# Kernel tuning notes

Measured on AMD Instinct MI355X. Metric: run time of the kernel, lower is better.

The kernel has to match this reference:

```python
import jax, jax.numpy as jnp
import numpy as np

EPS = 1e-5

def layer_norm(x, w):
    mu = jnp.mean(x, axis=-1, keepdims=True)
    var = jnp.mean((x - mu) ** 2, axis=-1, keepdims=True)
    return (x - mu) * jax.lax.rsqrt(var + EPS) * w

def timestep_embedding(t, dim=256, max_period=10000.0):
    half = dim // 2
    freqs = jnp.exp(-np.log(max_period) * jnp.arange(half, dtype=jnp.float32) / half)
    args = t[:, None].astype(jnp.float32) * freqs[None]
    return jnp.concatenate([jnp.cos(args), jnp.sin(args)], axis=-1)  # (B, dim)


def setup_inputs() -> dict:
    key = jax.random.key(0)
    ks = jax.random.split(key, 16)
    B, S, D, H, L, V, C, F = 2, 1024, 768, 12, 12, 50258, 768, 256
    MLP = 4 * D
    w = 0.02  # init scale for weights
    return {
        "indices": jax.random.randint(ks[0], (B, S), 0, V, dtype=jnp.int32),
        "sigma": jax.random.uniform(ks[1], (B,), dtype=jnp.float32),
        "embed": jax.random.normal(ks[2], (V, D), jnp.float32) * w,
        "t_w1": jax.random.normal(ks[3], (C, F), jnp.float32) * w,
        "t_b1": jnp.zeros((C,), jnp.float32),
        "t_w2": jax.random.normal(ks[4], (C, C), jnp.float32) * w,
        "t_b2": jnp.zeros((C,), jnp.float32),
        "norm1_w": jnp.ones((L, D), jnp.float32),
        "qkv_w": jax.random.normal(ks[5], (L, 3 * D, D), jnp.float32) * w,
        "out_w": jax.random.normal(ks[6], (L, D, D), jnp.float32) * w,
        "norm2_w": jnp.ones((L, D), jnp.float32),
        "mlp_w1": jax.random.normal(ks[7], (L, MLP, D), jnp.float32) * w,
        "mlp_b1": jnp.zeros((L, MLP), jnp.float32),
        "mlp_w2": jax.random.normal(ks[8], (L, D, MLP), jnp.float32) * w,
        "mlp_b2": jnp.zeros((L, D), jnp.float32),
        "ada_w": jax.random.normal(ks[9], (L, 6 * D, C), jnp.float32) * w,
        "ada_b": jnp.zeros((L, 6 * D), jnp.float32),
        "normf_w": jnp.ones((D,), jnp.float32),
        "lin_w": jax.random.normal(ks[10], (V, D), jnp.float32) * w,
        "lin_b": jnp.zeros((V,), jnp.float32),
        "adaf_w": jax.random.normal(ks[11], (2 * D, C), jnp.float32) * w,
        "adaf_b": jnp.zeros((2 * D,), jnp.float32),
    }


def reference(indices, sigma, embed, t_w1, t_b1, t_w2, t_b2, norm1_w, qkv_w,
              out_w, norm2_w, mlp_w1, mlp_b1, mlp_w2, mlp_b2, ada_w, ada_b,
              normf_w, lin_w, lin_b, adaf_w, adaf_b):
    B, S = indices.shape
    D = embed.shape[1]
    L = qkv_w.shape[0]
    H = 12
    dh = D // H
    scale = 1.0 / np.sqrt(dh)

    x = embed[indices]  # (B, S, D)
    # conditioning: c = silu(MLP(sinusoidal(sigma)))
    tf = timestep_embedding(sigma)
    temb = jax.nn.silu(tf @ t_w1.T + t_b1) @ t_w2.T + t_b2
    c = jax.nn.silu(temb)  # (B, C)

    # NOTE: rotary cos/sin are computed but never applied in the original block.
    for l in range(L):
        ada = (c @ ada_w[l].T + ada_b[l]).reshape(B, 6, 1, D)
        sh_msa, sc_msa, g_msa = ada[:, 0], ada[:, 1], ada[:, 2]  # (B, 1, D)
        sh_mlp, sc_mlp, g_mlp = ada[:, 3], ada[:, 4], ada[:, 5]

        xm = layer_norm(x, norm1_w[l]) * (1 + sc_msa) + sh_msa
        qkv = (xm @ qkv_w[l].T).reshape(B, S, 3, H, dh)
        q, k, v = qkv[:, :, 0], qkv[:, :, 1], qkv[:, :, 2]  # (B, S, H, dh)
        attn = jnp.einsum('bqhd,bkhd->bhqk', q, k) * scale
        attn = jax.nn.softmax(attn, axis=-1)
        o = jnp.einsum('bhqk,bkhd->bqhd', attn, v).reshape(B, S, D)
        x = x + g_msa * (o @ out_w[l].T)

        xm = layer_norm(x, norm2_w[l]) * (1 + sc_mlp) + sh_mlp
        h = jax.nn.gelu(xm @ mlp_w1[l].T + mlp_b1[l], approximate=True)
        x = x + g_mlp * (h @ mlp_w2[l].T + mlp_b2[l])

    ada = (c @ adaf_w.T + adaf_b).reshape(B, 2, 1, D)
    shift, sc = ada[:, 0], ada[:, 1]
    xm = layer_norm(x, normf_w) * (1 + sc) + shift
    return xm @ lin_w.T + lin_b  # (B, S, V) log-scores
```

## Files before the change

### kernel.cpp

```cpp
#include <hip/hip_runtime.h>
#include <hip/hip_bf16.h>
#include <math.h>
#include <stdint.h>

typedef __hip_bfloat16 bf16;
typedef __attribute__((ext_vector_type(8))) short bf16x8;
typedef __attribute__((ext_vector_type(4))) float f32x4;

#define DEV_INLINE __device__ __forceinline__

DEV_INLINE float wred_sum(float v) {
    #pragma unroll
    for (int o = 32; o > 0; o >>= 1) v += __shfl_xor(v, o);
    return v;
}
DEV_INLINE float red16_max(float v) {
    v = fmaxf(v, __shfl_xor(v, 1)); v = fmaxf(v, __shfl_xor(v, 2));
    v = fmaxf(v, __shfl_xor(v, 4)); v = fmaxf(v, __shfl_xor(v, 8));
    return v;
}
DEV_INLINE float red16_sum(float v) {
    v += __shfl_xor(v, 1); v += __shfl_xor(v, 2);
    v += __shfl_xor(v, 4); v += __shfl_xor(v, 8);
    return v;
}
DEV_INLINE float gelu_tanh(float v) {
    float t = tanhf(0.7978845608028654f * (v + 0.044715f * v * v * v));
    return 0.5f * v * (1.f + t);
}
DEV_INLINE float silu(float v) { return v / (1.f + expf(-v)); }
DEV_INLINE short f2bs(float f) { bf16 h = __float2bfloat16(f); short s; __builtin_memcpy(&s, &h, 2); return s; }

typedef const __attribute__((address_space(1))) uint32_t* gptr_t;
typedef __attribute__((address_space(3))) uint32_t* lptr_t;

DEV_INLINE void gload_lds16(const bf16* gp, bf16* lp) {
    __builtin_amdgcn_global_load_lds((gptr_t)gp, (lptr_t)lp, 16, 0, 0);
}

DEV_INLINE int xcd_swz(int wg, int nwg) {
    int q = nwg >> 3, r = nwg & 7;
    int xcd = wg & 7, pos = wg >> 3;
    return (xcd < r ? xcd * (q + 1) : r * (q + 1) + (xcd - r) * q) + pos;
}

__global__ void cvt_bf16(const float* __restrict__ in, bf16* __restrict__ out, long n) {
    long i = ((long)blockIdx.x * blockDim.x + threadIdx.x) * 8;
    if (i >= n) return;
    float4 a = *(const float4*)(in + i);
    float4 b = *(const float4*)(in + i + 4);
    bf16x8 v;
    v[0] = f2bs(a.x); v[1] = f2bs(a.y); v[2] = f2bs(a.z); v[3] = f2bs(a.w);
    v[4] = f2bs(b.x); v[5] = f2bs(b.y); v[6] = f2bs(b.z); v[7] = f2bs(b.w);
    *(bf16x8*)(out + i) = v;
}

__global__ void embed_gather(const int* __restrict__ idx,
                             const float* __restrict__ embed,
                             float* __restrict__ x) {
    int i = blockIdx.x * blockDim.x + threadIdx.x;
    int m = i / 192, d4 = i % 192;
    ((float4*)x)[(size_t)m * 192 + d4] =
        ((const float4*)embed)[(size_t)idx[m] * 192 + d4];
}

__global__ void tstep_embed(const float* __restrict__ sigma, float* __restrict__ tf) {
    int t = threadIdx.x;
    int b = t >> 7, i = t & 127;
    float freq = expf(-9.210340371976184f * (float)i / 128.f);
    float a = sigma[b] * freq;
    tf[b * 256 + i]       = cosf(a);
    tf[b * 256 + 128 + i] = sinf(a);
}

template <int ACT>
__global__ void gemm_rowvec(const float* __restrict__ A, const float* __restrict__ W,
                            const float* __restrict__ bias, float* __restrict__ C,
                            int M, int N, int K) {
    int wid  = (int)((blockIdx.x * (size_t)blockDim.x + threadIdx.x) >> 6);
    int lane = threadIdx.x & 63;
    if (wid >= M * N) return;
    int m = wid / N, n = wid % N;
    const float* a = A + (size_t)m * K;
    const float* w = W + (size_t)n * K;
    float s = 0.f;
    for (int k = lane; k < K; k += 64) s = fmaf(a[k], w[k], s);
    s = wred_sum(s);
    if (lane == 0) {
        if (bias) s += bias[n];
        if (ACT == 2) s = silu(s);
        C[wid] = s;
    }
}

__global__ void ada_all(const float* __restrict__ c, const float* __restrict__ ada_w,
                        const float* __restrict__ ada_b, float* __restrict__ out) {
    const int C = 768, SIXD = 4608, B = 2;
    int wid  = (int)((blockIdx.x * (size_t)blockDim.x + threadIdx.x) >> 6);
    int lane = threadIdx.x & 63;
    if (wid >= 12 * B * SIXD) return;
    int j = wid % SIXD;
    int lb = wid / SIXD;
    int b = lb % B, l = lb / B;
    const float* a = c + (size_t)b * C;
    const float* w = ada_w + ((size_t)l * SIXD + j) * C;
    float s = 0.f;
    for (int k = lane; k < C; k += 64) s = fmaf(a[k], w[k], s);
    s = wred_sum(s);
    if (lane == 0) out[wid] = s + ada_b[l * SIXD + j];
}

__global__ __launch_bounds__(256) void ln_mod(const float* __restrict__ x,
                                              const float* __restrict__ w,
                                              const float* __restrict__ sc,
                                              const float* __restrict__ sh,
                                              int bstride,
                                              bf16* __restrict__ out) {
    int r = blockIdx.x;
    int b = r >> 10;
    const float* xr = x + (size_t)r * 768;
    int tid = threadIdx.x, lane = tid & 63, wv = tid >> 6;
    float v0 = xr[tid], v1 = xr[tid + 256], v2 = xr[tid + 512];
    __shared__ float redA[4], redB[4];
    float s = wred_sum(v0 + v1 + v2);
    if (lane == 0) redA[wv] = s;
    __syncthreads();
    float mu = (redA[0] + redA[1] + redA[2] + redA[3]) * (1.f / 768.f);
    float d0 = v0 - mu, d1 = v1 - mu, d2 = v2 - mu;
    float vs = wred_sum(d0 * d0 + d1 * d1 + d2 * d2);
    if (lane == 0) redB[wv] = vs;
    __syncthreads();
    float var  = (redB[0] + redB[1] + redB[2] + redB[3]) * (1.f / 768.f);
    float rstd = rsqrtf(var + 1e-5f);
    const float* scb = sc + (size_t)b * bstride;
    const float* shb = sh + (size_t)b * bstride;
    bf16* outr = out + (size_t)r * 768;
    outr[tid]       = __float2bfloat16(d0 * rstd * w[tid]       * (1.f + scb[tid])       + shb[tid]);
    outr[tid + 256] = __float2bfloat16(d1 * rstd * w[tid + 256] * (1.f + scb[tid + 256]) + shb[tid + 256]);
    outr[tid + 512] = __float2bfloat16(d2 * rstd * w[tid + 512] * (1.f + scb[tid + 512]) + shb[tid + 512]);
}

template <int NPART>
__global__ __launch_bounds__(256) void ln_mod_red(float* __restrict__ x,
                                                  const float* __restrict__ part,
                                                  const float* __restrict__ bias,
                                                  const float* __restrict__ gate,
                                                  int gst,
                                                  const float* __restrict__ w,
                                                  const float* __restrict__ sc,
                                                  const float* __restrict__ sh,
                                                  int bstride,
                                                  bf16* __restrict__ out) {
    const size_t PST = (size_t)2048 * 768;
    int r = blockIdx.x;
    int b = r >> 10;
    float* xr = x + (size_t)r * 768;
    int tid = threadIdx.x, lane = tid & 63, wv = tid >> 6;

    float v[3];
    #pragma unroll
    for (int e = 0; e < 3; e++) {
        int d = tid + e * 256;
        float s0 = 0.f;
        #pragma unroll
        for (int p = 0; p < NPART; p++) s0 += part[(size_t)p * PST + (size_t)r * 768 + d];
        if (bias) s0 += bias[d];
        v[e] = xr[d] + gate[b * gst + d] * s0;
        xr[d] = v[e];
    }

    __shared__ float redA[4], redB[4];
    float s = wred_sum(v[0] + v[1] + v[2]);
    if (lane == 0) redA[wv] = s;
    __syncthreads();
    float mu = (redA[0] + redA[1] + redA[2] + redA[3]) * (1.f / 768.f);
    float d0 = v[0] - mu, d1 = v[1] - mu, d2 = v[2] - mu;
    float vs = wred_sum(d0 * d0 + d1 * d1 + d2 * d2);
    if (lane == 0) redB[wv] = vs;
    __syncthreads();
    float var  = (redB[0] + redB[1] + redB[2] + redB[3]) * (1.f / 768.f);
    float rstd = rsqrtf(var + 1e-5f);
    const float* scb = sc + (size_t)b * bstride;
    const float* shb = sh + (size_t)b * bstride;
    bf16* outr = out + (size_t)r * 768;
    outr[tid]       = __float2bfloat16(d0 * rstd * w[tid]       * (1.f + scb[tid])       + shb[tid]);
    outr[tid + 256] = __float2bfloat16(d1 * rstd * w[tid + 256] * (1.f + scb[tid + 256]) + shb[tid + 256]);
    outr[tid + 512] = __float2bfloat16(d2 * rstd * w[tid + 512] * (1.f + scb[tid + 512]) + shb[tid + 512]);
}

template <int ACT, int OMODE, int SK>
__global__ __launch_bounds__(256) void gemm_mfma(const bf16* __restrict__ A,
                                                 const bf16* __restrict__ W,
                                                 const float* __restrict__ bias,
                                                 void* __restrict__ Cout,
                                                 bf16* __restrict__ vtout,
                                                 int M, int N, int K) {
    __shared__ __align__(16) bf16 SA[2][128 * 32];
    __shared__ __align__(16) bf16 SW[2][128 * 32];
    int tid = threadIdx.x;
    int w = tid >> 6, l = tid & 63;
    int l16 = l & 15, g = l >> 4;
    int wgid = xcd_swz(blockIdx.x, gridDim.x);
    int MT = M >> 7;
    int nt = gridDim.x / (MT * SK);
    int m0 = (wgid % MT) * 128;
    int n  = (wgid / MT) % nt;
    int s  = wgid / (MT * nt);
    int n0 = n * 128;
    int kb = K / SK;
    int k0 = s * kb;
    int wr = (w >> 1) * 64, wc = (w & 1) * 64;

    f32x4 acc[4][4];
    f32x4 zero4 = {0.f, 0.f, 0.f, 0.f};
    #pragma unroll
    for (int i = 0; i < 4; i++)
        #pragma unroll
        for (int j = 0; j < 4; j++) acc[i][j] = zero4;

    int srow = w * 32 + (l >> 2);
    int scol = ((l & 3) ^ ((l >> 3) & 3)) * 8;
    const bf16* gA0 = A + (size_t)(m0 + srow) * K + k0 + scol;
    const bf16* gA1 = gA0 + (size_t)16 * K;
    int nr0 = n0 + srow;      if (nr0 > N - 1) nr0 = N - 1;
    int nr1 = n0 + srow + 16; if (nr1 > N - 1) nr1 = N - 1;
    const bf16* gW0 = W + (size_t)nr0 * K + k0 + scol;
    const bf16* gW1 = W + (size_t)nr1 * K + k0 + scol;
    int ldsA0 = (w * 32) * 32, ldsA1 = (w * 32 + 16) * 32;

    int sA = (g ^ ((l16 >> 1) & 3)) * 8;

    gload_lds16(gA0, &SA[0][ldsA0]);
    gload_lds16(gA1, &SA[0][ldsA1]);
    gload_lds16(gW0, &SW[0][ldsA0]);
    gload_lds16(gW1, &SW[0][ldsA1]);
    __syncthreads();

    int cur = 0;
    for (int kk = 0; kk < kb; kk += 32) {
        if (kk + 32 < kb) {
            int nb = cur ^ 1;
            gload_lds16(gA0 + kk + 32, &SA[nb][ldsA0]);
            gload_lds16(gA1 + kk + 32, &SA[nb][ldsA1]);
            gload_lds16(gW0 + kk + 32, &SW[nb][ldsA0]);
            gload_lds16(gW1 + kk + 32, &SW[nb][ldsA1]);
        }
        bf16x8 af[4], bfr[4];
        #pragma unroll
        for (int mi = 0; mi < 4; mi++)
            af[mi] = *(const bf16x8*)&SA[cur][(wr + mi * 16 + l16) * 32 + sA];
        #pragma unroll
        for (int ni = 0; ni < 4; ni++)
            bfr[ni] = *(const bf16x8*)&SW[cur][(wc + ni * 16 + l16) * 32 + sA];
        #pragma unroll
        for (int mi = 0; mi < 4; mi++)
            #pragma unroll
            for (int ni = 0; ni < 4; ni++)
                acc[mi][ni] = __builtin_amdgcn_mfma_f32_16x16x32_bf16(
                    af[mi], bfr[ni], acc[mi][ni], 0, 0, 0);
        __syncthreads();
        cur ^= 1;
    }

    if (OMODE == 3 && n0 >= 1536) {
        #pragma unroll
        for (int ni = 0; ni < 4; ni++) {
            int cv = n0 + wc + ni * 16 + l16 - 1536;
            int h = cv >> 6, d = cv & 63;
            #pragma unroll
            for (int mi = 0; mi < 4; mi++) {
                int row = m0 + wr + mi * 16 + g * 4;
                int b = row >> 10, ss = row & 1023;
                short4 pk;
                pk.x = f2bs(acc[mi][ni][0]); pk.y = f2bs(acc[mi][ni][1]);
                pk.z = f2bs(acc[mi][ni][2]); pk.w = f2bs(acc[mi][ni][3]);
                *(short4*)&vtout[(((size_t)(b * 12 + h) * 64 + d)) * 1024 + ss] = pk;
            }
        }
        return;
    }
    float* pout = (OMODE == 4) ? (float*)Cout + (size_t)s * M * N : (float*)Cout;
    #pragma unroll
    for (int ni = 0; ni < 4; ni++) {
        int col = n0 + wc + ni * 16 + l16;
        if (col >= N) continue;
        float bv = (OMODE != 4 && bias) ? bias[col] : 0.f;
        #pragma unroll
        for (int mi = 0; mi < 4; mi++) {
            #pragma unroll
            for (int jj = 0; jj < 4; jj++) {
                int row = m0 + wr + mi * 16 + g * 4 + jj;
                float v = acc[mi][ni][jj] + bv;
                if (ACT == 1) v = gelu_tanh(v);
                if (OMODE == 1 || OMODE == 3) {
                    ((bf16*)Cout)[(size_t)row * N + col] = __float2bfloat16(v);
                } else {
                    pout[(size_t)row * N + col] = v;
                }
            }
        }
    }
}

__global__ __launch_bounds__(256) void attn_mfma(const bf16* __restrict__ qkv,
                                                 const bf16* __restrict__ vt,
                                                 bf16* __restrict__ ao) {
    const int S = 1024, C3 = 2304;
    int wgid = xcd_swz(blockIdx.x, gridDim.x);
    int bh = wgid >> 4, b = bh / 12, h = bh % 12;
    int q0 = (wgid & 15) * 64;
    int tid = threadIdx.x, w = tid >> 6, l = tid & 63;
    int l16 = l & 15, g = l >> 4;

    __shared__ __align__(16) bf16 Ks[2][64 * 64];
    __shared__ __align__(16) bf16 Vs[2][64 * 64];
    __shared__ __align__(16) bf16 Ps[4][16 * 72];

    const size_t qbase = ((size_t)(b * S + q0 + w * 16 + l16)) * C3 + h * 64;
    bf16x8 qf[2];
    qf[0] = *(const bf16x8*)&qkv[qbase + g * 8];
    qf[1] = *(const bf16x8*)&qkv[qbase + 32 + g * 8];

    f32x4 o_acc[4];
    f32x4 zero4 = {0.f, 0.f, 0.f, 0.f};
    #pragma unroll
    for (int ni = 0; ni < 4; ni++) o_acc[ni] = zero4;
    float mrow[4] = {-1e30f, -1e30f, -1e30f, -1e30f};
    float lrow[4] = {0.f, 0.f, 0.f, 0.f};
    const float cscale = 0.125f * 1.44269504088896f;

    int sr0 = w * 16 + (l >> 3);
    int sr1 = sr0 + 8;
    int cb  = (l & 7) * 16;
    int sc0 = (cb ^ ((sr0 & 7) << 4)) >> 1;
    int sc1 = (cb ^ ((sr1 & 7) << 4)) >> 1;
    const bf16* gk0 = qkv + ((size_t)(b * S) + sr0) * C3 + 768 + h * 64 + sc0;
    const bf16* gk1 = qkv + ((size_t)(b * S) + sr1) * C3 + 768 + h * 64 + sc1;
    const bf16* gv0 = vt + ((size_t)bh * 64 + sr0) * 1024 + sc0;
    const bf16* gv1 = vt + ((size_t)bh * 64 + sr1) * 1024 + sc1;
    int ldk0 = (w * 16) * 64, ldk1 = (w * 16 + 8) * 64;

    gload_lds16(gk0, &Ks[0][ldk0]);
    gload_lds16(gk1, &Ks[0][ldk1]);
    gload_lds16(gv0, &Vs[0][ldk0]);
    gload_lds16(gv1, &Vs[0][ldk1]);
    __syncthreads();

    int cur = 0;
    for (int kv0 = 0; kv0 < S; kv0 += 64) {
        if (kv0 + 64 < S) {
            int nb = cur ^ 1;
            gload_lds16(gk0 + (size_t)(kv0 + 64) * C3, &Ks[nb][ldk0]);
            gload_lds16(gk1 + (size_t)(kv0 + 64) * C3, &Ks[nb][ldk1]);
            gload_lds16(gv0 + kv0 + 64, &Vs[nb][ldk0]);
            gload_lds16(gv1 + kv0 + 64, &Vs[nb][ldk1]);
        }

        f32x4 sfrag[4];
        #pragma unroll
        for (int kf = 0; kf < 4; kf++) {
            sfrag[kf] = zero4;
            int key = kf * 16 + l16;
            #pragma unroll
            for (int kc = 0; kc < 2; kc++) {
                int byteoff = key * 128 + (((kc * 32 + g * 8) * 2) ^ ((key & 7) << 4));
                bf16x8 kb = *(const bf16x8*)((const char*)Ks[cur] + byteoff);
                sfrag[kf] = __builtin_amdgcn_mfma_f32_16x16x32_bf16(qf[kc], kb, sfrag[kf], 0, 0, 0);
            }
        }

        float pv[4][4];
        #pragma unroll
        for (int j = 0; j < 4; j++) {
            float t0 = sfrag[0][j] * cscale, t1 = sfrag[1][j] * cscale;
            float t2 = sfrag[2][j] * cscale, t3 = sfrag[3][j] * cscale;
            float mx = fmaxf(fmaxf(t0, t1), fmaxf(t2, t3));
            mx = red16_max(mx);
            float mnew = fmaxf(mrow[j], mx);
            float r = exp2f(mrow[j] - mnew);
            mrow[j] = mnew;
            float p0 = exp2f(t0 - mnew), p1 = exp2f(t1 - mnew);
            float p2 = exp2f(t2 - mnew), p3 = exp2f(t3 - mnew);
            pv[0][j] = p0; pv[1][j] = p1; pv[2][j] = p2; pv[3][j] = p3;
            float ps = red16_sum(p0 + p1 + p2 + p3);
            lrow[j] = lrow[j] * r + ps;
            #pragma unroll
            for (int ni = 0; ni < 4; ni++) o_acc[ni][j] *= r;
        }

        #pragma unroll
        for (int kf = 0; kf < 4; kf++)
            #pragma unroll
            for (int j = 0; j < 4; j++)
                Ps[w][(g * 4 + j) * 72 + kf * 16 + l16] = __float2bfloat16(pv[kf][j]);

        #pragma unroll
        for (int kc = 0; kc < 2; kc++) {
            bf16x8 pa = *(const bf16x8*)&Ps[w][l16 * 72 + kc * 32 + g * 8];
            #pragma unroll
            for (int ni = 0; ni < 4; ni++) {
                int d = ni * 16 + l16;
                int byteoff = d * 128 + (((kc * 32 + g * 8) * 2) ^ ((d & 7) << 4));
                bf16x8 vb = *(const bf16x8*)((const char*)Vs[cur] + byteoff);
                o_acc[ni] = __builtin_amdgcn_mfma_f32_16x16x32_bf16(pa, vb, o_acc[ni], 0, 0, 0);
            }
        }
        __syncthreads();
        cur ^= 1;
    }

    float linv[4];
    #pragma unroll
    for (int j = 0; j < 4; j++) linv[j] = 1.f / lrow[j];
    #pragma unroll
    for (int ni = 0; ni < 4; ni++) {
        #pragma unroll
        for (int jj = 0; jj < 4; jj++) {
            int row = q0 + w * 16 + g * 4 + jj;
            ao[((size_t)(b * S + row)) * 768 + h * 64 + ni * 16 + l16] =
                __float2bfloat16(o_acc[ni][jj] * linv[jj]);
        }
    }
}

extern "C" void kernel_launch(void* const* d_in, const int* in_sizes, int n_in,
                              void* d_out, int out_size, void* d_ws, size_t ws_size,
                              hipStream_t stream) {
    const int B = 2, S = 1024, D = 768, L = 12, V = 50258, C = 768, F = 256, MLP = 3072;
    const int M = B * S;

    const int*   indices = (const int*)d_in[0];
    const float* sigma   = (const float*)d_in[1];
    const float* embed   = (const float*)d_in[2];
    const float* t_w1    = (const float*)d_in[3];
    const float* t_b1    = (const float*)d_in[4];
    const float* t_w2    = (const float*)d_in[5];
    const float* t_b2    = (const float*)d_in[6];
    const float* norm1_w = (const float*)d_in[7];
    const float* qkv_w   = (const float*)d_in[8];
    const float* out_w   = (const float*)d_in[9];
    const float* norm2_w = (const float*)d_in[10];
    const float* mlp_w1  = (const float*)d_in[11];
    const float* mlp_b1  = (const float*)d_in[12];
    const float* mlp_w2  = (const float*)d_in[13];
    const float* mlp_b2  = (const float*)d_in[14];
    const float* ada_w   = (const float*)d_in[15];
    const float* ada_b   = (const float*)d_in[16];
    const float* normf_w = (const float*)d_in[17];
    const float* lin_w   = (const float*)d_in[18];
    const float* lin_b   = (const float*)d_in[19];
    const float* adaf_w  = (const float*)d_in[20];
    const float* adaf_b  = (const float*)d_in[21];

    char* p = (char*)d_ws;
    auto alloc = [&](size_t bytes) { char* r = p; p += (bytes + 255) & ~(size_t)255; return r; };

    float* x     = (float*)alloc((size_t)M * D * 4);
    bf16*  xm    = (bf16*) alloc((size_t)M * D * 2);
    bf16*  qkvb  = (bf16*) alloc((size_t)M * 3 * D * 2);
    bf16*  aob   = (bf16*) alloc((size_t)M * D * 2);
    bf16*  hbb   = (bf16*) alloc((size_t)M * MLP * 2);
    bf16*  vtb   = (bf16*) alloc((size_t)24 * 64 * 1024 * 2);
    float* partb = (float*)alloc((size_t)4 * M * D * 4);
    bf16*  linb  = (bf16*) alloc((size_t)V * D * 2);
    float* tf    = (float*)alloc((size_t)B * F * 4);
    float* h1    = (float*)alloc((size_t)B * C * 4);
    float* cb    = (float*)alloc((size_t)B * C * 4);
    float* ada   = (float*)alloc((size_t)L * B * 6 * D * 4);
    float* adaf  = (float*)alloc((size_t)B * 2 * D * 4);

    const size_t n_qkvw = (size_t)L * 2304 * 768;
    const size_t n_outw = (size_t)L * 768 * 768;
    const size_t n_w1   = (size_t)L * 3072 * 768;
    const size_t n_w2   = (size_t)L * 768 * 3072;
    const size_t per_layer = (size_t)(2304 + 768 + 3072 + 3072) * 768;
    size_t used = (size_t)(p - (char*)d_ws);
    bool all_w = (ws_size - used) >= ((n_qkvw + n_outw + n_w1 + n_w2) * 2 + 1024);

    bf16 *wqkv, *wout, *ww1, *ww2;
    if (all_w) {
        wqkv = (bf16*)alloc(n_qkvw * 2);
        wout = (bf16*)alloc(n_outw * 2);
        ww1  = (bf16*)alloc(n_w1 * 2);
        ww2  = (bf16*)alloc(n_w2 * 2);
    } else {
        bf16* wl = (bf16*)alloc(per_layer * 2);
        wqkv = wl;
        wout = wqkv + (size_t)2304 * 768;
        ww1  = wout + (size_t)768 * 768;
        ww2  = ww1 + (size_t)3072 * 768;
    }

    auto cgrid = [](long n) { return (unsigned)((n / 8 + 255) / 256); };
    dim3 blk(256);

    embed_gather<<<(M * 192) / 256, blk, 0, stream>>>(indices, embed, x);
    tstep_embed<<<1, blk, 0, stream>>>(sigma, tf);
    gemm_rowvec<2><<<(B * C * 64) / 256, blk, 0, stream>>>(tf, t_w1, t_b1, h1, B, C, F);
    gemm_rowvec<2><<<(B * C * 64) / 256, blk, 0, stream>>>(h1, t_w2, t_b2, cb, B, C, C);
    ada_all<<<(L * B * 6 * D * 64) / 256, blk, 0, stream>>>(cb, ada_w, ada_b, ada);
    gemm_rowvec<0><<<(B * 2 * D * 64) / 256, blk, 0, stream>>>(cb, adaf_w, adaf_b, adaf, B, 2 * D, C);
    cvt_bf16<<<cgrid((long)V * D), blk, 0, stream>>>(lin_w, linb, (long)V * D);
    if (all_w) {
        cvt_bf16<<<cgrid((long)n_qkvw), blk, 0, stream>>>(qkv_w, wqkv, (long)n_qkvw);
        cvt_bf16<<<cgrid((long)n_outw), blk, 0, stream>>>(out_w, wout, (long)n_outw);
        cvt_bf16<<<cgrid((long)n_w1),   blk, 0, stream>>>(mlp_w1, ww1, (long)n_w1);
        cvt_bf16<<<cgrid((long)n_w2),   blk, 0, stream>>>(mlp_w2, ww2, (long)n_w2);
    }

    const int MT = M / 128;
    for (int l = 0; l < L; l++) {
        const float* adaL = ada + (size_t)l * B * 6 * D;
        bf16 *wq, *wo, *w1, *w2;
        if (all_w) {
            wq = wqkv + (size_t)l * 2304 * 768;
            wo = wout + (size_t)l * 768 * 768;
            w1 = ww1 + (size_t)l * 3072 * 768;
            w2 = ww2 + (size_t)l * 768 * 3072;
        } else {
            wq = wqkv; wo = wout; w1 = ww1; w2 = ww2;
            cvt_bf16<<<cgrid((long)2304 * 768), blk, 0, stream>>>(qkv_w + (size_t)l * 2304 * 768, wq, (long)2304 * 768);
            cvt_bf16<<<cgrid((long)768 * 768),  blk, 0, stream>>>(out_w + (size_t)l * 768 * 768,  wo, (long)768 * 768);
            cvt_bf16<<<cgrid((long)3072 * 768), blk, 0, stream>>>(mlp_w1 + (size_t)l * 3072 * 768, w1, (long)3072 * 768);
            cvt_bf16<<<cgrid((long)768 * 3072), blk, 0, stream>>>(mlp_w2 + (size_t)l * 768 * 3072, w2, (long)768 * 3072);
        }

        if (l == 0) {
            ln_mod<<<M, blk, 0, stream>>>(x, norm1_w, adaL + D, adaL, 6 * D, xm);
        } else {
            const float* adaP = ada + (size_t)(l - 1) * B * 6 * D;
            ln_mod_red<4><<<M, blk, 0, stream>>>(
                x, partb, mlp_b2 + (size_t)(l - 1) * D, adaP + 5 * D, 6 * D,
                norm1_w + (size_t)l * D, adaL + D, adaL, 6 * D, xm);
        }

        gemm_mfma<0, 3, 1><<<MT * (2304 / 128), blk, 0, stream>>>(
            xm, wq, nullptr, qkvb, vtb, M, 2304, 768);
        attn_mfma<<<384, blk, 0, stream>>>(qkvb, vtb, aob);
        gemm_mfma<0, 4, 2><<<MT * (768 / 128) * 2, blk, 0, stream>>>(
            aob, wo, nullptr, partb, nullptr, M, 768, 768);
        ln_mod_red<2><<<M, blk, 0, stream>>>(
            x, partb, nullptr, adaL + 2 * D, 6 * D,
            norm2_w + (size_t)l * D, adaL + 4 * D, adaL + 3 * D, 6 * D, xm);

        gemm_mfma<1, 1, 1><<<MT * (3072 / 128), blk, 0, stream>>>(
            xm, w1, mlp_b1 + (size_t)l * MLP, hbb, nullptr, M, 3072, 768);
        gemm_mfma<0, 4, 4><<<MT * (768 / 128) * 4, blk, 0, stream>>>(
            hbb, w2, nullptr, partb, nullptr, M, 768, 3072);
    }

    {
        const float* adaP = ada + (size_t)(L - 1) * B * 6 * D;
        ln_mod_red<4><<<M, blk, 0, stream>>>(
            x, partb, mlp_b2 + (size_t)(L - 1) * D, adaP + 5 * D, 6 * D,
            normf_w, adaf + D, adaf, 2 * D, xm);
    }
    gemm_mfma<0, 0, 1><<<MT * ((V + 127) / 128), blk, 0, stream>>>(
        xm, linb, lin_b, (float*)d_out, nullptr, M, V, 768);
}
```

Baseline: 2.361 ms.

## Triple-buffer LDS staging in GEMM and attention with one barrier per iteration

Both the GEMM and attention kernels go from double-buffered to triple-buffered LDS tiles and prefetch two tiles ahead. The trailing __syncthreads is replaced by a single inline-asm wait (vmcnt(4), or vmcnt(0) on the last iteration) plus barrier at the top of each iteration. This keeps more global loads in flight and removes one barrier per step. In exchange it uses more LDS, which may lower occupancy. It also depends on the hand-written vmcnt counts being correct, and in attention the Ps scratch buffer is no longer protected by the end-of-loop barrier.

Result: no change. 2.351 ms (-0.4%).

```diff
diff --git a/kernel.cpp b/kernel.cpp
--- a/kernel.cpp
+++ b/kernel.cpp
@@ -37,6 +37,9 @@
 DEV_INLINE void gload_lds16(const bf16* gp, bf16* lp) {
     __builtin_amdgcn_global_load_lds((gptr_t)gp, (lptr_t)lp, 16, 0, 0);
 }
+
+#define WAITBAR4() asm volatile("s_waitcnt vmcnt(4)\ns_barrier" ::: "memory")
+#define WAITBAR0() asm volatile("s_waitcnt vmcnt(0)\ns_barrier" ::: "memory")
 
 DEV_INLINE int xcd_swz(int wg, int nwg) {
     int q = nwg >> 3, r = nwg & 7;
@@ -195,8 +198,8 @@
                                                  void* __restrict__ Cout,
                                                  bf16* __restrict__ vtout,
                                                  int M, int N, int K) {
-    __shared__ __align__(16) bf16 SA[2][128 * 32];
-    __shared__ __align__(16) bf16 SW[2][128 * 32];
+    __shared__ __align__(16) bf16 SA[3][128 * 32];
+    __shared__ __align__(16) bf16 SW[3][128 * 32];
     int tid = threadIdx.x;
     int w = tid >> 6, l = tid & 63;
     int l16 = l & 15, g = l >> 4;
@@ -230,36 +233,34 @@
 
     int sA = (g ^ ((l16 >> 1) & 3)) * 8;
 
-    gload_lds16(gA0, &SA[0][ldsA0]);
-    gload_lds16(gA1, &SA[0][ldsA1]);
-    gload_lds16(gW0, &SW[0][ldsA0]);
-    gload_lds16(gW1, &SW[0][ldsA1]);
-    __syncthreads();
-
-    int cur = 0;
-    for (int kk = 0; kk < kb; kk += 32) {
-        if (kk + 32 < kb) {
-            int nb = cur ^ 1;
-            gload_lds16(gA0 + kk + 32, &SA[nb][ldsA0]);
-            gload_lds16(gA1 + kk + 32, &SA[nb][ldsA1]);
-            gload_lds16(gW0 + kk + 32, &SW[nb][ldsA0]);
-            gload_lds16(gW1 + kk + 32, &SW[nb][ldsA1]);
-        }
+    auto STAGE = [&](int kk, int bufi) {
+        gload_lds16(gA0 + kk, &SA[bufi][ldsA0]);
+        gload_lds16(gA1 + kk, &SA[bufi][ldsA1]);
+        gload_lds16(gW0 + kk, &SW[bufi][ldsA0]);
+        gload_lds16(gW1 + kk, &SW[bufi][ldsA1]);
+    };
+
+    int KT = kb >> 5;
+    STAGE(0, 0);
+    if (KT > 1) STAGE(32, 1);
+
+    for (int k = 0; k < KT; ++k) {
+        if (k == KT - 1) { WAITBAR0(); } else { WAITBAR4(); }
+        if (k + 2 < KT) STAGE((k + 2) * 32, (k + 2) % 3);
+        int cbuf = k % 3;
         bf16x8 af[4], bfr[4];
         #pragma unroll
         for (int mi = 0; mi < 4; mi++)
-            af[mi] = *(const bf16x8*)&SA[cur][(wr + mi * 16 + l16) * 32 + sA];
+            af[mi] = *(const bf16x8*)&SA[cbuf][(wr + mi * 16 + l16) * 32 + sA];
         #pragma unroll
         for (int ni = 0; ni < 4; ni++)
-            bfr[ni] = *(const bf16x8*)&SW[cur][(wc + ni * 16 + l16) * 32 + sA];
+            bfr[ni] = *(const bf16x8*)&SW[cbuf][(wc + ni * 16 + l16) * 32 + sA];
         #pragma unroll
         for (int mi = 0; mi < 4; mi++)
             #pragma unroll
             for (int ni = 0; ni < 4; ni++)
                 acc[mi][ni] = __builtin_amdgcn_mfma_f32_16x16x32_bf16(
                     af[mi], bfr[ni], acc[mi][ni], 0, 0, 0);
-        __syncthreads();
-        cur ^= 1;
     }
 
     if (OMODE == 3 && n0 >= 1536) {
@@ -312,8 +313,8 @@
     int tid = threadIdx.x, w = tid >> 6, l = tid & 63;
     int l16 = l & 15, g = l >> 4;
 
-    __shared__ __align__(16) bf16 Ks[2][64 * 64];
-    __shared__ __align__(16) bf16 Vs[2][64 * 64];
+    __shared__ __align__(16) bf16 Ks[3][64 * 64];
+    __shared__ __align__(16) bf16 Vs[3][64 * 64];
     __shared__ __align__(16) bf16 Ps[4][16 * 72];
 
     const size_t qbase = ((size_t)(b * S + q0 + w * 16 + l16)) * C3 + h * 64;
@@ -340,21 +341,20 @@
     const bf16* gv1 = vt + ((size_t)bh * 64 + sr1) * 1024 + sc1;
     int ldk0 = (w * 16) * 64, ldk1 = (w * 16 + 8) * 64;
 
-    gload_lds16(gk0, &Ks[0][ldk0]);
-    gload_lds16(gk1, &Ks[0][ldk1]);
-    gload_lds16(gv0, &Vs[0][ldk0]);
-    gload_lds16(gv1, &Vs[0][ldk1]);
-    __syncthreads();
-
-    int cur = 0;
-    for (int kv0 = 0; kv0 < S; kv0 += 64) {
-        if (kv0 + 64 < S) {
-            int nb = cur ^ 1;
-            gload_lds16(gk0 + (size_t)(kv0 + 64) * C3, &Ks[nb][ldk0]);
-            gload_lds16(gk1 + (size_t)(kv0 + 64) * C3, &Ks[nb][ldk1]);
-            gload_lds16(gv0 + kv0 + 64, &Vs[nb][ldk0]);
-            gload_lds16(gv1 + kv0 + 64, &Vs[nb][ldk1]);
-        }
+    auto STAGEKV = [&](int t, int bufi) {
+        gload_lds16(gk0 + (size_t)(t * 64) * C3, &Ks[bufi][ldk0]);
+        gload_lds16(gk1 + (size_t)(t * 64) * C3, &Ks[bufi][ldk1]);
+        gload_lds16(gv0 + t * 64, &Vs[bufi][ldk0]);
+        gload_lds16(gv1 + t * 64, &Vs[bufi][ldk1]);
+    };
+
+    STAGEKV(0, 0);
+    STAGEKV(1, 1);
+
+    for (int it = 0; it < 16; ++it) {
+        if (it == 15) { WAITBAR0(); } else { WAITBAR4(); }
+        if (it + 2 < 16) STAGEKV(it + 2, (it + 2) % 3);
+        int cur = it % 3;
 
         f32x4 sfrag[4];
         #pragma unroll
@@ -405,8 +405,6 @@
                 o_acc[ni] = __builtin_amdgcn_mfma_f32_16x16x32_bf16(pa, vb, o_acc[ni], 0, 0, 0);
             }
         }
-        __syncthreads();
-        cur ^= 1;
     }
 
     float linv[4];
```
